# Kernel tuning notes

Hardware: AMD Instinct MI355X
Metric: run time of the kernel (lower is better)

The kernel has to match this reference:

```python
import jax, jax.numpy as jnp
import numpy as np

B, T, D_IN, H, L = 256, 1024, 64, 1024, 3
ALPHA = 0.5        # leaking_rate
SPECTRAL = 0.9     # spectral_radius


def setup_inputs() -> dict:
    key = jax.random.key(0)
    k0, k1, k2, k3, k4 = jax.random.split(key, 5)
    x = jax.random.normal(k0, (B, T, D_IN), dtype=jnp.float32)
    # Fixed reservoir weights. W_res is scaled so its spectral radius is ~SPECTRAL
    # (randn(H,H)/sqrt(H) has spectral radius ~1 for large H, matching the
    # eigvals-based normalization done at torch init time).
    W_in0 = jax.random.normal(k1, (H, D_IN), dtype=jnp.float32) * 0.1
    W_in_rest = jax.random.normal(k2, (L - 1, H, H), dtype=jnp.float32) * 0.1
    W_res = jax.random.normal(k3, (L, H, H), dtype=jnp.float32) * (SPECTRAL / np.sqrt(H))
    kw, kb = jax.random.split(k4)
    # readout: Linear(H*L, 1), torch default uniform(-1/sqrt(fan_in), 1/sqrt(fan_in))
    bound = 1.0 / np.sqrt(H * L)
    w_out = jax.random.uniform(kw, (1, H * L), minval=-bound, maxval=bound, dtype=jnp.float32)
    b_out = jax.random.uniform(kb, (1,), minval=-bound, maxval=bound, dtype=jnp.float32)
    return {"x": x, "W_in0": W_in0, "W_in_rest": W_in_rest, "W_res": W_res,
            "w_out": w_out, "b_out": b_out}


def reference(x, W_in0, W_in_rest, W_res, w_out, b_out):
    # x: [B, T, D_IN]; states carried as [L, B, H]
    def step(states, x_t):
        cur = x_t  # [B, D_in] then [B, H] for deeper layers
        new_states = []
        for i in range(L):
            W_in = W_in0 if i == 0 else W_in_rest[i - 1]
            pre = cur @ W_in.T + states[i] @ W_res[i].T  # [B, H]
            h = (1.0 - ALPHA) * states[i] + ALPHA * jnp.tanh(pre)
            new_states.append(h)
            cur = h
        return jnp.stack(new_states), None

    init = jnp.zeros((L, B, H), dtype=x.dtype)
    final_states, _ = jax.lax.scan(step, init, jnp.swapaxes(x, 0, 1))  # scan over T
    # torch.cat(states, dim=1): layer-major concat -> [B, L*H]
    feat = jnp.transpose(final_states, (1, 0, 2)).reshape(B, L * H)
    out = feat @ w_out.T + b_out  # [B, 1]
    return out.squeeze(-1)
```

## Files before the change

### kernel.cpp

```cpp
#include <hip/hip_runtime.h>
#include <hip/hip_bf16.h>

#define BB 256
#define TT 1024
#define DIN 64
#define HH 1024
#define NL 3
#define ALPHA 0.5f
#define SBUF (NL * BB * HH)
#define NWG 192

typedef __attribute__((ext_vector_type(8))) short bf16x8;
typedef __attribute__((ext_vector_type(4))) float f32x4;
typedef __attribute__((ext_vector_type(4))) unsigned short u16x4;

static const size_t XT_OFF  = 0;
static const size_t WB_OFF  = 33554432;
static const size_t S16_OFF = 44171264;
static const size_t S32_OFF = 47316992;
static const size_t BAR_OFF = 50462720;

#define WIN0_E   0
#define WIN12_E  65536
#define WRES_E   2162688

__global__ void convert_kernel(const float* __restrict__ w_in0,
                               const float* __restrict__ w_in_rest,
                               const float* __restrict__ w_res,
                               __hip_bfloat16* __restrict__ Wb)
{
    const size_t total = 65536ull + 2097152ull + 3145728ull;
    for (size_t i = (size_t)blockIdx.x * blockDim.x + threadIdx.x; i < total;
         i += (size_t)gridDim.x * blockDim.x) {
        float v;
        if (i < 65536)            v = w_in0[i];
        else if (i < 2162688)     v = w_in_rest[i - 65536];
        else                      v = w_res[i - 2162688];
        Wb[i] = __float2bfloat16(v);
    }
}

__global__ void transpose_x_kernel(const float* __restrict__ x,
                                   unsigned short* __restrict__ xT)
{
    const size_t n4 = (size_t)BB * TT * DIN / 4;
    for (size_t i = (size_t)blockIdx.x * blockDim.x + threadIdx.x; i < n4;
         i += (size_t)gridDim.x * blockDim.x) {
        size_t flat = i * 4;
        int d = (int)(flat & (DIN - 1));
        int t = (int)((flat >> 6) & (TT - 1));
        int b = (int)(flat >> 16);
        const float4 v = reinterpret_cast<const float4*>(x)[i];
        __hip_bfloat16 h0 = __float2bfloat16(v.x);
        __hip_bfloat16 h1 = __float2bfloat16(v.y);
        __hip_bfloat16 h2 = __float2bfloat16(v.z);
        __hip_bfloat16 h3 = __float2bfloat16(v.w);
        u16x4 pk;
        pk.x = *(unsigned short*)&h0; pk.y = *(unsigned short*)&h1;
        pk.z = *(unsigned short*)&h2; pk.w = *(unsigned short*)&h3;
        *reinterpret_cast<u16x4*>(xT + ((size_t)t * BB + b) * DIN + d) = pk;
    }
}

__device__ __forceinline__ float tanh_fast(float x) {
    float e = __expf(2.0f * x);
    return 1.0f - 2.0f / (e + 1.0f);
}

__device__ __forceinline__ void grid_barrier(unsigned int* __restrict__ bar, int step)
{
    __syncthreads();
    if (threadIdx.x == 0) {
        const unsigned int want = (unsigned int)(step + 1);
        unsigned int old = __hip_atomic_fetch_add(bar, 1u, __ATOMIC_RELEASE,
                                                  __HIP_MEMORY_SCOPE_AGENT);
        if (old == (unsigned int)NWG * want - 1u) {
            __hip_atomic_store(bar + 32, want, __ATOMIC_RELEASE,
                               __HIP_MEMORY_SCOPE_AGENT);
        } else {
            while (__hip_atomic_load(bar + 32, __ATOMIC_RELAXED,
                                     __HIP_MEMORY_SCOPE_AGENT) < want)
                __builtin_amdgcn_s_sleep(2);
        }
        __builtin_amdgcn_fence(__ATOMIC_ACQUIRE, "agent");
    }
    __syncthreads();
}

template <int KTOT>
__device__ __forceinline__ void gemm_lds(const unsigned short* __restrict__ A0,
                                         const unsigned short* __restrict__ A1,
                                         const char* __restrict__ Bp,
                                         f32x4& a00, f32x4& a01, f32x4& a10, f32x4& a11)
{
#pragma unroll 8
    for (int k = 0; k < KTOT; k += 32) {
        bf16x8 a0 = *(const bf16x8*)(A0 + k);
        bf16x8 a1 = *(const bf16x8*)(A1 + k);
        bf16x8 b0 = *(const bf16x8*)(Bp + k * 64);
        bf16x8 b1 = *(const bf16x8*)(Bp + k * 64 + 256);
        a00 = __builtin_amdgcn_mfma_f32_16x16x32_bf16(a0, b0, a00, 0, 0, 0);
        a01 = __builtin_amdgcn_mfma_f32_16x16x32_bf16(a0, b1, a01, 0, 0, 0);
        a10 = __builtin_amdgcn_mfma_f32_16x16x32_bf16(a1, b0, a10, 0, 0, 0);
        a11 = __builtin_amdgcn_mfma_f32_16x16x32_bf16(a1, b1, a11, 0, 0, 0);
    }
}

__global__ __launch_bounds__(256, 1) void esn_main(
    const unsigned short* __restrict__ xT,
    const unsigned short* __restrict__ Wb,
    unsigned short* __restrict__ S16,
    float* __restrict__ S32,
    unsigned int* __restrict__ bar)
{
    __shared__ char Blds[131072];

    const int wg  = blockIdx.x;
    const int bi  = wg / 96;
    const int rem = wg - bi * 96;
    const int l   = rem >> 5;
    const int ni  = rem & 31;
    const int n0  = ni * 32;

    const int tid  = threadIdx.x;
    const int lane = tid & 63;
    const int w    = tid >> 6;

    {
        const unsigned short* gWin = (l == 0) ? (Wb + WIN0_E)
                                              : (Wb + WIN12_E + (size_t)(l - 1) * HH * HH);
        const int kin  = (l == 0) ? DIN : HH;
        const int nblk = 32 * (kin >> 3);
        for (int idx = tid; idx < nblk; idx += 256) {
            int c   = idx & 31;
            int kb8 = idx >> 5;
            bf16x8 v = *(const bf16x8*)(gWin + (size_t)(n0 + c) * kin + kb8 * 8);
            *(bf16x8*)(Blds + (kb8 * 32 + c) * 16) = v;
        }
        const unsigned short* gWres = Wb + WRES_E + (size_t)l * HH * HH;
        for (int idx = tid; idx < 32 * 128; idx += 256) {
            int c   = idx & 31;
            int kb8 = idx >> 5;
            bf16x8 v = *(const bf16x8*)(gWres + (size_t)(n0 + c) * HH + kb8 * 8);
            *(bf16x8*)(Blds + 65536 + (kb8 * 32 + c) * 16) = v;
        }
    }
    __syncthreads();

    const int ar = lane & 15;
    const int kq = (lane >> 4) << 3;
    const int m0 = bi * 128 + w * 32;
    const char* BpIn  = Blds + ((kq >> 3) * 32 + ar) * 16;
    const char* BpRes = BpIn + 65536;
    const int rb = (lane >> 4) << 2;
    const int cc = lane & 15;

    float mst[2][2][4];
#pragma unroll
    for (int i = 0; i < 2; ++i)
#pragma unroll
        for (int j = 0; j < 2; ++j)
#pragma unroll
            for (int r = 0; r < 4; ++r) mst[i][j][r] = 0.f;

    for (int s = 0; s < TT + NL - 1; ++s) {
        const int t = s - l;
        const unsigned short* Sc = S16 + (size_t)(s & 1) * SBUF;
        unsigned short*       Sn = S16 + (size_t)((s + 1) & 1) * SBUF;
        if (t >= 0 && t < TT) {
            f32x4 a00 = {0.f, 0.f, 0.f, 0.f};
            f32x4 a01 = a00, a10 = a00, a11 = a00;
            {
                const unsigned short* A  = Sc + (size_t)l * (BB * HH);
                const unsigned short* A0 = A + (size_t)(m0 + ar) * HH + kq;
                gemm_lds<HH>(A0, A0 + 16 * HH, BpRes, a00, a01, a10, a11);
            }
            if (l == 0) {
                const unsigned short* A  = xT + (size_t)t * (BB * DIN);
                const unsigned short* A0 = A + (size_t)(m0 + ar) * DIN + kq;
                gemm_lds<DIN>(A0, A0 + 16 * DIN, BpIn, a00, a01, a10, a11);
            } else {
                const unsigned short* A  = Sc + (size_t)(l - 1) * (BB * HH);
                const unsigned short* A0 = A + (size_t)(m0 + ar) * HH + kq;
                gemm_lds<HH>(A0, A0 + 16 * HH, BpIn, a00, a01, a10, a11);
            }
#pragma unroll
            for (int i = 0; i < 2; ++i)
#pragma unroll
            for (int j = 0; j < 2; ++j) {
                f32x4 acc = (i == 0) ? ((j == 0) ? a00 : a01) : ((j == 0) ? a10 : a11);
#pragma unroll
                for (int r = 0; r < 4; ++r) {
                    float hnew = (1.0f - ALPHA) * mst[i][j][r] + ALPHA * tanh_fast(acc[r]);
                    mst[i][j][r] = hnew;
                    int b = m0 + i * 16 + rb + r;
                    int h = n0 + j * 16 + cc;
                    __hip_bfloat16 hb = __float2bfloat16(hnew);
                    Sn[((size_t)l * BB + b) * HH + h] = *(unsigned short*)&hb;
                }
            }
        }
        grid_barrier(bar, s);
    }

#pragma unroll
    for (int i = 0; i < 2; ++i)
#pragma unroll
    for (int j = 0; j < 2; ++j)
#pragma unroll
    for (int r = 0; r < 4; ++r) {
        int b = m0 + i * 16 + rb + r;
        int h = n0 + j * 16 + cc;
        S32[((size_t)l * BB + b) * HH + h] = mst[i][j][r];
    }
}

__global__ void out_kernel(const float* __restrict__ S32,
                           const float* __restrict__ w_out,
                           const float* __restrict__ b_out,
                           float* __restrict__ out)
{
    int b = blockIdx.x;
    int tid = threadIdx.x;
    float p = 0.f;
    for (int idx = tid; idx < NL * HH; idx += 256) {
        int l = idx >> 10;
        int h = idx & (HH - 1);
        p += S32[((size_t)l * BB + b) * HH + h] * w_out[idx];
    }
    __shared__ float red[256];
    red[tid] = p;
    __syncthreads();
    for (int off = 128; off > 0; off >>= 1) {
        if (tid < off) red[tid] += red[tid + off];
        __syncthreads();
    }
    if (tid == 0) out[b] = red[0] + b_out[0];
}

extern "C" void kernel_launch(void* const* d_in, const int* in_sizes, int n_in,
                              void* d_out, int out_size, void* d_ws, size_t ws_size,
                              hipStream_t stream)
{
    const float* x         = (const float*)d_in[0];
    const float* W_in0     = (const float*)d_in[1];
    const float* W_in_rest = (const float*)d_in[2];
    const float* W_res     = (const float*)d_in[3];
    const float* w_out     = (const float*)d_in[4];
    const float* b_out     = (const float*)d_in[5];

    char* ws = (char*)d_ws;
    const unsigned short* xTp  = (const unsigned short*)(ws + XT_OFF);
    __hip_bfloat16*       Wbh  = (__hip_bfloat16*)(ws + WB_OFF);
    const unsigned short* Wbp  = (const unsigned short*)(ws + WB_OFF);
    unsigned short*       S16p = (unsigned short*)(ws + S16_OFF);
    float*                S32p = (float*)(ws + S32_OFF);
    unsigned int*         barp = (unsigned int*)(ws + BAR_OFF);

    convert_kernel<<<4096, 256, 0, stream>>>(W_in0, W_in_rest, W_res, Wbh);
    transpose_x_kernel<<<4096, 256, 0, stream>>>(x, (unsigned short*)(ws + XT_OFF));
    hipMemsetAsync(ws + S16_OFF, 0, 6291712, stream);

    void* args[] = { (void*)&xTp, (void*)&Wbp, (void*)&S16p, (void*)&S32p, (void*)&barp };
    hipLaunchCooperativeKernel((const void*)esn_main, dim3(NWG), dim3(256),
                               args, 0, stream);

    out_kernel<<<BB, 256, 0, stream>>>(S32p, w_out, b_out, (float*)d_out);
}
```

Measured before the change: 27.90 ms.

## Double the waves per workgroup and register-prefetch state rows in fused dual GEMM

Each workgroup now runs 512 threads (8 waves), with each wave owning 16 batch rows instead of 32. The recurrent and input GEMMs for layers 1 and 2 are interleaved in one loop that double-buffers A-operand global loads in registers, so load latency is hidden behind MFMA work on the sequential critical path. Layer 0 reads fp32 x directly and converts it to bf16 in-kernel, which removes the separate transpose kernel and its workspace. The costs are higher register pressure and scattered, uncoalesced fp32 x reads on every timestep.

```diff
diff --git a/kernel.cpp b/kernel.cpp
--- a/kernel.cpp
+++ b/kernel.cpp
@@ -12,13 +12,11 @@
 
 typedef __attribute__((ext_vector_type(8))) short bf16x8;
 typedef __attribute__((ext_vector_type(4))) float f32x4;
-typedef __attribute__((ext_vector_type(4))) unsigned short u16x4;
-
-static const size_t XT_OFF  = 0;
-static const size_t WB_OFF  = 33554432;
-static const size_t S16_OFF = 44171264;
-static const size_t S32_OFF = 47316992;
-static const size_t BAR_OFF = 50462720;
+
+static const size_t WB_OFF  = 0;
+static const size_t S16_OFF = 10617344;
+static const size_t S32_OFF = 13763072;
+static const size_t BAR_OFF = 16908800;
 
 #define WIN0_E   0
 #define WIN12_E  65536
@@ -40,31 +38,19 @@
     }
 }
 
-__global__ void transpose_x_kernel(const float* __restrict__ x,
-                                   unsigned short* __restrict__ xT)
-{
-    const size_t n4 = (size_t)BB * TT * DIN / 4;
-    for (size_t i = (size_t)blockIdx.x * blockDim.x + threadIdx.x; i < n4;
-         i += (size_t)gridDim.x * blockDim.x) {
-        size_t flat = i * 4;
-        int d = (int)(flat & (DIN - 1));
-        int t = (int)((flat >> 6) & (TT - 1));
-        int b = (int)(flat >> 16);
-        const float4 v = reinterpret_cast<const float4*>(x)[i];
-        __hip_bfloat16 h0 = __float2bfloat16(v.x);
-        __hip_bfloat16 h1 = __float2bfloat16(v.y);
-        __hip_bfloat16 h2 = __float2bfloat16(v.z);
-        __hip_bfloat16 h3 = __float2bfloat16(v.w);
-        u16x4 pk;
-        pk.x = *(unsigned short*)&h0; pk.y = *(unsigned short*)&h1;
-        pk.z = *(unsigned short*)&h2; pk.w = *(unsigned short*)&h3;
-        *reinterpret_cast<u16x4*>(xT + ((size_t)t * BB + b) * DIN + d) = pk;
-    }
-}
-
 __device__ __forceinline__ float tanh_fast(float x) {
     float e = __expf(2.0f * x);
     return 1.0f - 2.0f / (e + 1.0f);
+}
+
+__device__ __forceinline__ bf16x8 cvt_pack8(const float* p) {
+    union { unsigned short s[8]; bf16x8 v; } x;
+#pragma unroll
+    for (int i = 0; i < 8; ++i) {
+        __hip_bfloat16 h = __float2bfloat16(p[i]);
+        x.s[i] = *(unsigned short*)&h;
+    }
+    return x.v;
 }
 
 __device__ __forceinline__ void grid_barrier(unsigned int* __restrict__ bar, int step)
@@ -87,27 +73,71 @@
     __syncthreads();
 }
 
-template <int KTOT>
-__device__ __forceinline__ void gemm_lds(const unsigned short* __restrict__ A0,
-                                         const unsigned short* __restrict__ A1,
-                                         const char* __restrict__ Bp,
-                                         f32x4& a00, f32x4& a01, f32x4& a10, f32x4& a11)
-{
-#pragma unroll 8
-    for (int k = 0; k < KTOT; k += 32) {
-        bf16x8 a0 = *(const bf16x8*)(A0 + k);
-        bf16x8 a1 = *(const bf16x8*)(A1 + k);
-        bf16x8 b0 = *(const bf16x8*)(Bp + k * 64);
-        bf16x8 b1 = *(const bf16x8*)(Bp + k * 64 + 256);
-        a00 = __builtin_amdgcn_mfma_f32_16x16x32_bf16(a0, b0, a00, 0, 0, 0);
-        a01 = __builtin_amdgcn_mfma_f32_16x16x32_bf16(a0, b1, a01, 0, 0, 0);
-        a10 = __builtin_amdgcn_mfma_f32_16x16x32_bf16(a1, b0, a10, 0, 0, 0);
-        a11 = __builtin_amdgcn_mfma_f32_16x16x32_bf16(a1, b1, a11, 0, 0, 0);
-    }
-}
-
-__global__ __launch_bounds__(256, 1) void esn_main(
-    const unsigned short* __restrict__ xT,
+__device__ __forceinline__ void gemm_dual(const unsigned short* __restrict__ Ar,
+                                          const unsigned short* __restrict__ Ai,
+                                          const char* __restrict__ Bpr,
+                                          const char* __restrict__ Bpi,
+                                          f32x4& a00, f32x4& a01)
+{
+    bf16x8 br[2][4], bn[2][4];
+#pragma unroll
+    for (int c = 0; c < 4; ++c) {
+        br[0][c] = *(const bf16x8*)(Ar + c * 32);
+        bn[0][c] = *(const bf16x8*)(Ai + c * 32);
+    }
+#pragma unroll
+    for (int ch = 0; ch < 8; ++ch) {
+        const int cur = ch & 1;
+        if (ch < 7) {
+#pragma unroll
+            for (int c = 0; c < 4; ++c) {
+                br[cur ^ 1][c] = *(const bf16x8*)(Ar + ((ch + 1) * 4 + c) * 32);
+                bn[cur ^ 1][c] = *(const bf16x8*)(Ai + ((ch + 1) * 4 + c) * 32);
+            }
+        }
+#pragma unroll
+        for (int c = 0; c < 4; ++c) {
+            const int k = (ch * 4 + c) * 32;
+            bf16x8 b0 = *(const bf16x8*)(Bpr + k * 64);
+            bf16x8 b1 = *(const bf16x8*)(Bpr + k * 64 + 256);
+            a00 = __builtin_amdgcn_mfma_f32_16x16x32_bf16(br[cur][c], b0, a00, 0, 0, 0);
+            a01 = __builtin_amdgcn_mfma_f32_16x16x32_bf16(br[cur][c], b1, a01, 0, 0, 0);
+            bf16x8 c0 = *(const bf16x8*)(Bpi + k * 64);
+            bf16x8 c1 = *(const bf16x8*)(Bpi + k * 64 + 256);
+            a00 = __builtin_amdgcn_mfma_f32_16x16x32_bf16(bn[cur][c], c0, a00, 0, 0, 0);
+            a01 = __builtin_amdgcn_mfma_f32_16x16x32_bf16(bn[cur][c], c1, a01, 0, 0, 0);
+        }
+    }
+}
+
+__device__ __forceinline__ void gemm_single(const unsigned short* __restrict__ Ar,
+                                            const char* __restrict__ Bp,
+                                            f32x4& a00, f32x4& a01)
+{
+    bf16x8 buf[2][4];
+#pragma unroll
+    for (int c = 0; c < 4; ++c) buf[0][c] = *(const bf16x8*)(Ar + c * 32);
+#pragma unroll
+    for (int ch = 0; ch < 8; ++ch) {
+        const int cur = ch & 1;
+        if (ch < 7) {
+#pragma unroll
+            for (int c = 0; c < 4; ++c)
+                buf[cur ^ 1][c] = *(const bf16x8*)(Ar + ((ch + 1) * 4 + c) * 32);
+        }
+#pragma unroll
+        for (int c = 0; c < 4; ++c) {
+            const int k = (ch * 4 + c) * 32;
+            bf16x8 b0 = *(const bf16x8*)(Bp + k * 64);
+            bf16x8 b1 = *(const bf16x8*)(Bp + k * 64 + 256);
+            a00 = __builtin_amdgcn_mfma_f32_16x16x32_bf16(buf[cur][c], b0, a00, 0, 0, 0);
+            a01 = __builtin_amdgcn_mfma_f32_16x16x32_bf16(buf[cur][c], b1, a01, 0, 0, 0);
+        }
+    }
+}
+
+__global__ __launch_bounds__(512, 2) void esn_main(
+    const float* __restrict__ x,
     const unsigned short* __restrict__ Wb,
     unsigned short* __restrict__ S16,
     float* __restrict__ S32,
@@ -131,14 +161,14 @@
                                               : (Wb + WIN12_E + (size_t)(l - 1) * HH * HH);
         const int kin  = (l == 0) ? DIN : HH;
         const int nblk = 32 * (kin >> 3);
-        for (int idx = tid; idx < nblk; idx += 256) {
+        for (int idx = tid; idx < nblk; idx += 512) {
             int c   = idx & 31;
             int kb8 = idx >> 5;
             bf16x8 v = *(const bf16x8*)(gWin + (size_t)(n0 + c) * kin + kb8 * 8);
             *(bf16x8*)(Blds + (kb8 * 32 + c) * 16) = v;
         }
         const unsigned short* gWres = Wb + WRES_E + (size_t)l * HH * HH;
-        for (int idx = tid; idx < 32 * 128; idx += 256) {
+        for (int idx = tid; idx < 32 * 128; idx += 512) {
             int c   = idx & 31;
             int kb8 = idx >> 5;
             bf16x8 v = *(const bf16x8*)(gWres + (size_t)(n0 + c) * HH + kb8 * 8);
@@ -149,19 +179,19 @@
 
     const int ar = lane & 15;
     const int kq = (lane >> 4) << 3;
-    const int m0 = bi * 128 + w * 32;
+    const int m0 = bi * 128 + w * 16;
     const char* BpIn  = Blds + ((kq >> 3) * 32 + ar) * 16;
     const char* BpRes = BpIn + 65536;
     const int rb = (lane >> 4) << 2;
     const int cc = lane & 15;
 
-    float mst[2][2][4];
-#pragma unroll
-    for (int i = 0; i < 2; ++i)
-#pragma unroll
-        for (int j = 0; j < 2; ++j)
-#pragma unroll
-            for (int r = 0; r < 4; ++r) mst[i][j][r] = 0.f;
+    const size_t PLANE = (size_t)BB * HH;
+
+    float mst[2][4];
+#pragma unroll
+    for (int j = 0; j < 2; ++j)
+#pragma unroll
+        for (int r = 0; r < 4; ++r) mst[j][r] = 0.f;
 
     for (int s = 0; s < TT + NL - 1; ++s) {
         const int t = s - l;
@@ -169,31 +199,34 @@
         unsigned short*       Sn = S16 + (size_t)((s + 1) & 1) * SBUF;
         if (t >= 0 && t < TT) {
             f32x4 a00 = {0.f, 0.f, 0.f, 0.f};
-            f32x4 a01 = a00, a10 = a00, a11 = a00;
-            {
-                const unsigned short* A  = Sc + (size_t)l * (BB * HH);
-                const unsigned short* A0 = A + (size_t)(m0 + ar) * HH + kq;
-                gemm_lds<HH>(A0, A0 + 16 * HH, BpRes, a00, a01, a10, a11);
+            f32x4 a01 = a00;
+
+            if (l == 0) {
+                const unsigned short* Ar = Sc + (size_t)(m0 + ar) * HH + kq;
+                gemm_single(Ar, BpRes, a00, a01);
+                const float* xr = x + ((size_t)(m0 + ar) * TT + t) * DIN + kq;
+#pragma unroll
+                for (int k = 0; k < DIN; k += 32) {
+                    bf16x8 a0 = cvt_pack8(xr + k);
+                    bf16x8 b0 = *(const bf16x8*)(BpIn + k * 64);
+                    bf16x8 b1 = *(const bf16x8*)(BpIn + k * 64 + 256);
+                    a00 = __builtin_amdgcn_mfma_f32_16x16x32_bf16(a0, b0, a00, 0, 0, 0);
+                    a01 = __builtin_amdgcn_mfma_f32_16x16x32_bf16(a0, b1, a01, 0, 0, 0);
+                }
+            } else {
+                const unsigned short* Ar = Sc + (size_t)l * PLANE + (size_t)(m0 + ar) * HH + kq;
+                const unsigned short* Ai = Sc + (size_t)(l - 1) * PLANE + (size_t)(m0 + ar) * HH + kq;
+                gemm_dual(Ar, Ai, BpRes, BpIn, a00, a01);
             }
-            if (l == 0) {
-                const unsigned short* A  = xT + (size_t)t * (BB * DIN);
-                const unsigned short* A0 = A + (size_t)(m0 + ar) * DIN + kq;
-                gemm_lds<DIN>(A0, A0 + 16 * DIN, BpIn, a00, a01, a10, a11);
-            } else {
-                const unsigned short* A  = Sc + (size_t)(l - 1) * (BB * HH);
-                const unsigned short* A0 = A + (size_t)(m0 + ar) * HH + kq;
-                gemm_lds<HH>(A0, A0 + 16 * HH, BpIn, a00, a01, a10, a11);
-            }
-#pragma unroll
-            for (int i = 0; i < 2; ++i)
+
 #pragma unroll
             for (int j = 0; j < 2; ++j) {
-                f32x4 acc = (i == 0) ? ((j == 0) ? a00 : a01) : ((j == 0) ? a10 : a11);
+                f32x4 acc = (j == 0) ? a00 : a01;
 #pragma unroll
                 for (int r = 0; r < 4; ++r) {
-                    float hnew = (1.0f - ALPHA) * mst[i][j][r] + ALPHA * tanh_fast(acc[r]);
-                    mst[i][j][r] = hnew;
-                    int b = m0 + i * 16 + rb + r;
+                    float hnew = (1.0f - ALPHA) * mst[j][r] + ALPHA * tanh_fast(acc[r]);
+                    mst[j][r] = hnew;
+                    int b = m0 + rb + r;
                     int h = n0 + j * 16 + cc;
                     __hip_bfloat16 hb = __float2bfloat16(hnew);
                     Sn[((size_t)l * BB + b) * HH + h] = *(unsigned short*)&hb;
@@ -204,14 +237,12 @@
     }
 
 #pragma unroll
-    for (int i = 0; i < 2; ++i)
-#pragma unroll
     for (int j = 0; j < 2; ++j)
 #pragma unroll
     for (int r = 0; r < 4; ++r) {
-        int b = m0 + i * 16 + rb + r;
+        int b = m0 + rb + r;
         int h = n0 + j * 16 + cc;
-        S32[((size_t)l * BB + b) * HH + h] = mst[i][j][r];
+        S32[((size_t)l * BB + b) * HH + h] = mst[j][r];
     }
 }
 
@@ -250,7 +281,6 @@
     const float* b_out     = (const float*)d_in[5];
 
     char* ws = (char*)d_ws;
-    const unsigned short* xTp  = (const unsigned short*)(ws + XT_OFF);
     __hip_bfloat16*       Wbh  = (__hip_bfloat16*)(ws + WB_OFF);
     const unsigned short* Wbp  = (const unsigned short*)(ws + WB_OFF);
     unsigned short*       S16p = (unsigned short*)(ws + S16_OFF);
@@ -258,11 +288,10 @@
     unsigned int*         barp = (unsigned int*)(ws + BAR_OFF);
 
     convert_kernel<<<4096, 256, 0, stream>>>(W_in0, W_in_rest, W_res, Wbh);
-    transpose_x_kernel<<<4096, 256, 0, stream>>>(x, (unsigned short*)(ws + XT_OFF));
     hipMemsetAsync(ws + S16_OFF, 0, 6291712, stream);
 
-    void* args[] = { (void*)&xTp, (void*)&Wbp, (void*)&S16p, (void*)&S32p, (void*)&barp };
-    hipLaunchCooperativeKernel((const void*)esn_main, dim3(NWG), dim3(256),
+    void* args[] = { (void*)&x, (void*)&Wbp, (void*)&S16p, (void*)&S32p, (void*)&barp };
+    hipLaunchCooperativeKernel((const void*)esn_main, dim3(NWG), dim3(512),
                                args, 0, stream);
 
     out_kernel<<<BB, 256, 0, stream>>>(S32p, w_out, b_out, (float*)d_out);
```

Result: faster. 22.88 ms (-18.0%).
